# Kernel tuning notes

Hardware: AMD Instinct MI355X
Metric: run time of the kernel (lower is better)

The kernel has to match this reference:

```python
import jax, jax.numpy as jnp
import numpy as np

NUM_HEADS = 32
NUM_KV_HEADS = 8
NUM_GROUPS = NUM_HEADS // NUM_KV_HEADS  # 4
HEAD_DIM = 64
HIDDEN = 2048
ROPE_THETA = 10000.0


def rotate_half(x):
    half = x.shape[-1] // 2
    x1, x2 = x[..., :half], x[..., half:]
    return jnp.concatenate([-x2, x1], axis=-1)


def rope_cos_sin(seq_len, dtype):
    inv_freq = 1.0 / (ROPE_THETA ** (jnp.arange(0, HEAD_DIM, 2, dtype=jnp.float32) / HEAD_DIM))
    pos = jnp.arange(seq_len, dtype=jnp.float32)
    freqs = jnp.outer(pos, inv_freq)          # [S, HEAD_DIM/2]
    emb = jnp.concatenate([freqs, freqs], axis=-1)  # [S, HEAD_DIM]
    return jnp.cos(emb).astype(dtype), jnp.sin(emb).astype(dtype)


def setup_inputs() -> dict:
    key = jax.random.key(0)
    k0, k1, k2, k3, k4 = jax.random.split(key, 5)
    B, S = 2, 2048
    scale = 0.02
    return {
        "hidden_states": jax.random.normal(k0, (B, S, HIDDEN), dtype=jnp.float32),
        "Wq": jax.random.normal(k1, (NUM_HEADS * HEAD_DIM, HIDDEN), dtype=jnp.float32) * scale,
        "Wk": jax.random.normal(k2, (NUM_KV_HEADS * HEAD_DIM, HIDDEN), dtype=jnp.float32) * scale,
        "Wv": jax.random.normal(k3, (NUM_KV_HEADS * HEAD_DIM, HIDDEN), dtype=jnp.float32) * scale,
        "Wo": jax.random.normal(k4, (HIDDEN, NUM_HEADS * HEAD_DIM), dtype=jnp.float32) * scale,
    }


def reference(hidden_states, Wq, Wk, Wv, Wo):
    B, S, _ = hidden_states.shape
    # projections (nn.Linear: x @ W.T)
    q = (hidden_states @ Wq.T).reshape(B, S, NUM_HEADS, HEAD_DIM).transpose(0, 2, 1, 3)
    k = (hidden_states @ Wk.T).reshape(B, S, NUM_KV_HEADS, HEAD_DIM).transpose(0, 2, 1, 3)
    v = (hidden_states @ Wv.T).reshape(B, S, NUM_KV_HEADS, HEAD_DIM).transpose(0, 2, 1, 3)

    cos, sin = rope_cos_sin(S, q.dtype)  # [S, HEAD_DIM]
    cos = cos[None, None]                # [1,1,S,HEAD_DIM]
    sin = sin[None, None]
    q = q * cos + rotate_half(q) * sin
    k = k * cos + rotate_half(k) * sin

    # GQA: repeat kv heads to match query heads (repeat_interleave on head dim)
    k = jnp.repeat(k, NUM_GROUPS, axis=1)  # [B, NUM_HEADS, S, HEAD_DIM]
    v = jnp.repeat(v, NUM_GROUPS, axis=1)

    scale = 1.0 / jnp.sqrt(jnp.asarray(HEAD_DIM, dtype=q.dtype))
    scores = jnp.einsum('bhqd,bhkd->bhqk', q, k) * scale  # [B,H,S,S]
    causal = jnp.tril(jnp.ones((S, S), dtype=bool))
    scores = jnp.where(causal[None, None], scores, jnp.asarray(-jnp.inf, dtype=scores.dtype))
    attn = jax.nn.softmax(scores, axis=-1)
    out = jnp.einsum('bhqk,bhkd->bhqd', attn, v)           # [B,H,S,D]
    out = out.transpose(0, 2, 1, 3).reshape(B, S, NUM_HEADS * HEAD_DIM)
    return out @ Wo.T
```

## Files before the change

### kernel.cpp

```cpp
#include <hip/hip_runtime.h>

#define S_LEN 2048
#define BATCH 2
#define NH 32
#define NKV 8
#define HD 64
#define HID 2048
#define NTOK (BATCH * S_LEN)
#define NQKV 3072
#define SC_Q 0.18033688011112042f

typedef __attribute__((ext_vector_type(8))) __bf16 bf16x8;
typedef __attribute__((ext_vector_type(4))) float f32x4;

__device__ inline ushort f2b(float f) {
    union { float f; unsigned u; } x{f};
    unsigned r = (x.u + 0x7fff + ((x.u >> 16) & 1)) >> 16;
    return (ushort)r;
}
__device__ inline float b2f(ushort u) {
    union { unsigned u; float f; } x{(unsigned)u << 16};
    return x.f;
}
__device__ inline float ex2(float x) { return __builtin_amdgcn_exp2f(x); }

__global__ __launch_bounds__(256) void cvt_all(const float* __restrict__ hidden,
                                               const float* __restrict__ Wq,
                                               const float* __restrict__ Wk,
                                               const float* __restrict__ Wv,
                                               const float* __restrict__ Wo,
                                               ushort* __restrict__ hb,
                                               ushort* __restrict__ wqkv,
                                               ushort* __restrict__ wo) {
    int bid = blockIdx.x;
    const float* src;
    ushort* dst;
    int off;
    if (bid < 8192)        { src = hidden; dst = hb;                              off = bid; }
    else if (bid < 12288)  { src = Wq;     dst = wqkv;                            off = bid - 8192; }
    else if (bid < 13312)  { src = Wk;     dst = wqkv + (size_t)2048 * 2048;      off = bid - 12288; }
    else if (bid < 14336)  { src = Wv;     dst = wqkv + (size_t)2560 * 2048;      off = bid - 13312; }
    else                   { src = Wo;     dst = wo;                              off = bid - 14336; }
    size_t i = (size_t)off * 256 + threadIdx.x;
    float4 v = reinterpret_cast<const float4*>(src)[i];
    ushort4 o;
    o.x = f2b(v.x); o.y = f2b(v.y); o.z = f2b(v.z); o.w = f2b(v.w);
    reinterpret_cast<ushort4*>(dst)[i] = o;
}

__device__ inline void gl_lds16(const void* g, void* l) {
    __builtin_amdgcn_global_load_lds((const __attribute__((address_space(1))) void*)g,
                                     (__attribute__((address_space(3))) void*)l, 16, 0, 0);
}

template<int CF, int WF32, int ROUTE>
__global__ __launch_bounds__(512, 2) void gemm8p(const ushort* __restrict__ A,
                                                 const ushort* __restrict__ B,
                                                 void* __restrict__ C,
                                                 ushort* __restrict__ Kd,
                                                 ushort* __restrict__ Vd,
                                                 int M, int N, int K) {
    constexpr int BN = CF * 64;
    constexpr int ABYTES = 256 * 64 * 2;
    constexpr int BBYTES = BN * 64 * 2;
    __shared__ __align__(16) char lds[2][ABYTES + BBYTES];
    const int tid = threadIdx.x, lane = tid & 63, w = tid >> 6;
    const int wm = w >> 2, wn = w & 3, l15 = lane & 15, lg = lane >> 4;

    const int nbx = gridDim.x;
    int lid = blockIdx.y * nbx + blockIdx.x;
    const int cpx = (nbx * gridDim.y) >> 3;
    int swzb = (lid & 7) * cpx + (lid >> 3);
    const int m0 = (swzb / nbx) * 256, n0 = (swzb % nbx) * BN;

    const int srow = tid >> 3;
    const int scol = ((tid & 7) ^ (srow & 7)) * 8;
    const ushort* Ag = A + (size_t)(m0 + srow) * K + scol;
    const ushort* Bg = B + (size_t)(n0 + srow) * K + scol;

    auto stage = [&](int buf, int k0) {
        char* base = &lds[buf][0];
#pragma unroll
        for (int j = 0; j < 4; j++)
            gl_lds16(Ag + (size_t)(j * 64) * K + k0, base + (j * 64 + w * 8) * 128);
#pragma unroll
        for (int j = 0; j < CF; j++)
            gl_lds16(Bg + (size_t)(j * 64) * K + k0, base + ABYTES + (j * 64 + w * 8) * 128);
    };

    f32x4 acc[8][CF] = {};

    stage(0, 0);
    asm volatile("s_waitcnt vmcnt(0)" ::: "memory");
    __builtin_amdgcn_s_barrier();
    __builtin_amdgcn_sched_barrier(0);

    const int NT = K >> 6;
    const int sw = (l15 & 7) * 16;
    const int po0 = (lg * 16) ^ sw, po1 = (64 + lg * 16) ^ sw;

    for (int t = 0; t < NT; ++t) {
        const char* pa = &lds[t & 1][0] + (wm * 128 + l15) * 128;
        const char* pb = &lds[t & 1][ABYTES] + (wn * CF * 16 + l15) * 128;

        bf16x8 bf_[2][CF];
        bf16x8 a0[2][2];
#pragma unroll
        for (int j = 0; j < CF; j++) {
            bf_[0][j] = *(const bf16x8*)(pb + j * 2048 + po0);
            bf_[1][j] = *(const bf16x8*)(pb + j * 2048 + po1);
        }
#pragma unroll
        for (int i = 0; i < 2; i++) {
            a0[0][i] = *(const bf16x8*)(pa + i * 2048 + po0);
            a0[1][i] = *(const bf16x8*)(pa + i * 2048 + po1);
        }
        if (t + 1 < NT) stage((t + 1) & 1, (t + 1) << 6);
        __builtin_amdgcn_sched_barrier(0);
        __builtin_amdgcn_s_barrier();
        __builtin_amdgcn_sched_barrier(0);
        __builtin_amdgcn_s_setprio(1);
#pragma unroll
        for (int ks = 0; ks < 2; ks++)
#pragma unroll
            for (int i = 0; i < 2; i++)
#pragma unroll
                for (int j = 0; j < CF; j++)
                    acc[i][j] = __builtin_amdgcn_mfma_f32_16x16x32_bf16(a0[ks][i], bf_[ks][j], acc[i][j], 0, 0, 0);
        __builtin_amdgcn_s_setprio(0);

#pragma unroll
        for (int p = 1; p < 4; p++) {
            bf16x8 ap[2][2];
#pragma unroll
            for (int i = 0; i < 2; i++) {
                ap[0][i] = *(const bf16x8*)(pa + (p * 2 + i) * 2048 + po0);
                ap[1][i] = *(const bf16x8*)(pa + (p * 2 + i) * 2048 + po1);
            }
            __builtin_amdgcn_sched_barrier(0);
            __builtin_amdgcn_s_barrier();
            __builtin_amdgcn_sched_barrier(0);
            __builtin_amdgcn_s_setprio(1);
#pragma unroll
            for (int ks = 0; ks < 2; ks++)
#pragma unroll
                for (int i = 0; i < 2; i++)
#pragma unroll
                    for (int j = 0; j < CF; j++)
                        acc[p * 2 + i][j] = __builtin_amdgcn_mfma_f32_16x16x32_bf16(ap[ks][i], bf_[ks][j], acc[p * 2 + i][j], 0, 0, 0);
            __builtin_amdgcn_s_setprio(0);
        }

        asm volatile("s_waitcnt vmcnt(0)" ::: "memory");
        __builtin_amdgcn_s_barrier();
        __builtin_amdgcn_sched_barrier(0);
    }

    const int mr = m0 + wm * 128 + lg * 4;

    if (ROUTE) {
#pragma unroll
        for (int j = 0; j < CF; j++) {
            int cb = n0 + wn * CF * 16 + j * 16;
            ushort* dst;
            int dstride, colb;
            if (cb < 2048)      { dst = (ushort*)C; dstride = 2048; colb = cb + l15; }
            else if (cb < 2560) { dst = Kd;         dstride = 512;  colb = cb - 2048 + l15; }
            else                { dst = Vd;         dstride = 512;  colb = cb - 2560 + l15; }
#pragma unroll
            for (int i = 0; i < 8; i++)
#pragma unroll
                for (int r = 0; r < 4; r++)
                    dst[(size_t)(mr + i * 16 + r) * dstride + colb] = f2b(acc[i][j][r]);
        }
    } else {
#pragma unroll
        for (int i = 0; i < 8; i++)
#pragma unroll
            for (int j = 0; j < CF; j++)
#pragma unroll
                for (int r = 0; r < 4; r++) {
                    size_t row = mr + i * 16 + r, col = n0 + wn * CF * 16 + j * 16 + l15;
                    if (WF32) ((float*)C)[row * N + col] = acc[i][j][r];
                    else      ((ushort*)C)[row * N + col] = f2b(acc[i][j][r]);
                }
    }
}

__global__ __launch_bounds__(256) void rope_k(ushort* __restrict__ Qb, ushort* __restrict__ Kb) {
    int idx = blockIdx.x * 256 + threadIdx.x;
    int t = idx / 160, rem = idx - t * 160;
    int hh = rem >> 2, q8 = rem & 3;
    float pos = (float)(t & (S_LEN - 1));
    ushort* base = (hh < 32) ? Qb + (size_t)t * 2048 + hh * 64 + q8 * 8
                             : Kb + (size_t)t * 512 + (hh - 32) * 64 + q8 * 8;
    float sc = (hh < 32) ? SC_Q : 1.0f;
    ushort4 v0 = *(ushort4*)base, v1 = *(ushort4*)(base + 4);
    ushort4 u0 = *(ushort4*)(base + 32), u1 = *(ushort4*)(base + 36);
    ushort lo[8] = {v0.x, v0.y, v0.z, v0.w, v1.x, v1.y, v1.z, v1.w};
    ushort hi[8] = {u0.x, u0.y, u0.z, u0.w, u1.x, u1.y, u1.z, u1.w};
#pragma unroll
    for (int e = 0; e < 8; e++) {
        float f = ex2(-(float)(q8 * 8 + e) * 0.4152410118609203f);
        float sv, cv;
        __sincosf(pos * f, &sv, &cv);
        float x1 = b2f(lo[e]), x2 = b2f(hi[e]);
        lo[e] = f2b((x1 * cv - x2 * sv) * sc);
        hi[e] = f2b((x2 * cv + x1 * sv) * sc);
    }
    *(ushort4*)base        = make_ushort4(lo[0], lo[1], lo[2], lo[3]);
    *(ushort4*)(base + 4)  = make_ushort4(lo[4], lo[5], lo[6], lo[7]);
    *(ushort4*)(base + 32) = make_ushort4(hi[0], hi[1], hi[2], hi[3]);
    *(ushort4*)(base + 36) = make_ushort4(hi[4], hi[5], hi[6], hi[7]);
}

__global__ __launch_bounds__(256) void transpose_v(const ushort* __restrict__ V,
                                                   ushort* __restrict__ Vt) {
    __shared__ ushort tile[32][33];
    int bz = blockIdx.z, b = bz >> 3, kvh = bz & 7;
    int s0 = blockIdx.x * 32, d0 = blockIdx.y * 32;
    int tx = threadIdx.x & 31, ty = threadIdx.x >> 5;
#pragma unroll
    for (int i = 0; i < 4; i++)
        tile[ty + i * 8][tx] = V[(size_t)(b * S_LEN + s0 + ty + i * 8) * 512 + kvh * 64 + d0 + tx];
    __syncthreads();
#pragma unroll
    for (int i = 0; i < 4; i++)
        Vt[((size_t)((b * 8 + kvh) * 64 + d0 + ty + i * 8)) * S_LEN + s0 + tx] = tile[tx][ty + i * 8];
}

__global__ __launch_bounds__(256) void attn_k(const ushort* __restrict__ Q,
                                              const ushort* __restrict__ Kc,
                                              const ushort* __restrict__ Vt,
                                              ushort* __restrict__ O) {
    __shared__ __align__(16) ushort K_lds[3][4096];
    __shared__ __align__(16) ushort V_lds[3][4096];
    const int lane = threadIdx.x & 63, w = threadIdx.x >> 6;
    const int l15 = lane & 15, lg = lane >> 4;

    int lid = blockIdx.y * 8 + blockIdx.x;
    int swz = (lid & 7) * 64 + (lid >> 3);
    const int ps = swz & 7;
    const int bh = swz >> 3;
    const int b = bh >> 5, h = bh & 31, kvh = h >> 2;

    const ushort* kSrc[2];
    const ushort* vSrc[2];
    int dstU[2];
#pragma unroll
    for (int j = 0; j < 2; j++) {
        int u = w * 2 + j;
        int row = u * 8 + (lane >> 3);
        int po = (lane & 7) * 16;
        int fr = ((row & 3) | (((row >> 3) & 1) << 2)) << 4;
        int dus = (po ^ fr) >> 1;
        kSrc[j] = Kc + (size_t)(b * S_LEN + row) * 512 + kvh * 64 + dus;
        vSrc[j] = Vt + ((size_t)((b * 8 + kvh) * 64 + row)) * S_LEN + dus;
        dstU[j] = u * 512;
    }

    int fr_k = ((l15 & 3) | (((l15 >> 2) & 1) << 2)) << 4;
    int kbase = 1024 * (l15 >> 2) + 128 * (l15 & 3) + ((lg * 16) ^ (fr_k & 48));
    int k6 = (fr_k >> 6) & 1;
    int kb0 = kbase + 64 * k6, kb1 = kbase + 64 * (1 - k6);
    int fr_v = ((l15 & 3) | (((l15 >> 3) & 1) << 2)) << 4;
    int vbase = 128 * l15 + ((lg * 16) ^ (fr_v & 48));
    int v6 = (fr_v >> 6) & 1;
    int vb0 = vbase + 64 * v6, vb1 = vbase + 64 * (1 - v6);

    bf16x8 onesf;
#pragma unroll
    for (int i = 0; i < 8; i++) onesf[i] = (__bf16)1.0f;

    for (int half = 0; half < 2; ++half) {
        const int pp = half ? (15 - ps) : ps;
        const int q0A = pp * 128 + w * 16, q0B = q0A + 64;
        const int qrowA = q0A + l15, qrowB = q0B + l15;
        const int ktA = 2 * pp, ktB = 2 * pp + 1;

        const ushort* qpA = Q + (size_t)(b * S_LEN + qrowA) * HID + h * 64 + lg * 8;
        const ushort* qpB = Q + (size_t)(b * S_LEN + qrowB) * HID + h * 64 + lg * 8;
        bf16x8 qfA0 = *(const bf16x8*)qpA, qfA1 = *(const bf16x8*)(qpA + 32);
        bf16x8 qfB0 = *(const bf16x8*)qpB, qfB1 = *(const bf16x8*)(qpB + 32);
        asm volatile("s_waitcnt vmcnt(0)" ::: "memory");

        f32x4 aoA[4] = {}, aoB[4] = {};
        f32x4 lsumA = {}, lsumB = {};

        int i0 = 0, i1 = 1, i2 = 2;
#pragma unroll
        for (int j = 0; j < 2; j++) {
            gl_lds16(kSrc[j], &K_lds[0][dstU[j]]);
            gl_lds16(vSrc[j], &V_lds[0][dstU[j]]);
        }
#pragma unroll
        for (int j = 0; j < 2; j++) {
            gl_lds16(kSrc[j] + (size_t)64 * 512, &K_lds[1][dstU[j]]);
            gl_lds16(vSrc[j] + 64, &V_lds[1][dstU[j]]);
        }

        for (int kt = 0; kt <= ktB; ++kt) {
            const int kn = kt << 6;
            if (kt < ktB) asm volatile("s_waitcnt vmcnt(4)" ::: "memory");
            else          asm volatile("s_waitcnt vmcnt(0)" ::: "memory");
            __builtin_amdgcn_s_barrier();

            if (kt + 2 <= ktB) {
                const int kn2 = kn + 128;
#pragma unroll
                for (int j = 0; j < 2; j++) {
                    gl_lds16(kSrc[j] + (size_t)kn2 * 512, &K_lds[i2][dstU[j]]);
                    gl_lds16(vSrc[j] + kn2, &V_lds[i2][dstU[j]]);
                }
            }

            const char* Kt = (const char*)&K_lds[i0][0];
            const char* Vl = (const char*)&V_lds[i0][0];
            const bool aAct = (kt <= ktA);

            bf16x8 kf0[4], kf1[4];
#pragma unroll
            for (int kc = 0; kc < 4; kc++) {
                const int kcst = 4096 * (kc >> 1) + 512 * (kc & 1);
                kf0[kc] = *(const bf16x8*)(Kt + kb0 + kcst);
                kf1[kc] = *(const bf16x8*)(Kt + kb1 + kcst);
            }

            f32x4 sB[4], sA[4];
#pragma unroll
            for (int kc = 0; kc < 4; kc++) {
                f32x4 z = {};
                z = __builtin_amdgcn_mfma_f32_16x16x32_bf16(kf0[kc], qfB0, z, 0, 0, 0);
                z = __builtin_amdgcn_mfma_f32_16x16x32_bf16(kf1[kc], qfB1, z, 0, 0, 0);
                sB[kc] = z;
            }
            if (aAct) {
#pragma unroll
                for (int kc = 0; kc < 4; kc++) {
                    f32x4 z = {};
                    z = __builtin_amdgcn_mfma_f32_16x16x32_bf16(kf0[kc], qfA0, z, 0, 0, 0);
                    z = __builtin_amdgcn_mfma_f32_16x16x32_bf16(kf1[kc], qfA1, z, 0, 0, 0);
                    sA[kc] = z;
                }
            }

            if (kt == ktB) {
#pragma unroll
                for (int kc = 0; kc < 4; kc++)
#pragma unroll
                    for (int r = 0; r < 4; r++) {
                        int kv = kn + ((kc >> 1) << 5) + (lg << 3) + ((kc & 1) << 2) + r;
                        sB[kc][r] = (kv <= qrowB) ? sB[kc][r] : -INFINITY;
                    }
            }
            if (kt == ktA) {
#pragma unroll
                for (int kc = 0; kc < 4; kc++)
#pragma unroll
                    for (int r = 0; r < 4; r++) {
                        int kv = kn + ((kc >> 1) << 5) + (lg << 3) + ((kc & 1) << 2) + r;
                        sA[kc][r] = (kv <= qrowA) ? sA[kc][r] : -INFINITY;
                    }
            }

            bf16x8 pB0, pB1, pA0, pA1;
#pragma unroll
            for (int r = 0; r < 4; r++) {
                pB0[r]     = (__bf16)ex2(sB[0][r]);
                pB0[4 + r] = (__bf16)ex2(sB[1][r]);
                pB1[r]     = (__bf16)ex2(sB[2][r]);
                pB1[4 + r] = (__bf16)ex2(sB[3][r]);
            }
            if (aAct) {
#pragma unroll
                for (int r = 0; r < 4; r++) {
                    pA0[r]     = (__bf16)ex2(sA[0][r]);
                    pA0[4 + r] = (__bf16)ex2(sA[1][r]);
                    pA1[r]     = (__bf16)ex2(sA[2][r]);
                    pA1[4 + r] = (__bf16)ex2(sA[3][r]);
                }
            }

            lsumB = __builtin_amdgcn_mfma_f32_16x16x32_bf16(pB0, onesf, lsumB, 0, 0, 0);
            lsumB = __builtin_amdgcn_mfma_f32_16x16x32_bf16(pB1, onesf, lsumB, 0, 0, 0);
            if (aAct) {
                lsumA = __builtin_amdgcn_mfma_f32_16x16x32_bf16(pA0, onesf, lsumA, 0, 0, 0);
                lsumA = __builtin_amdgcn_mfma_f32_16x16x32_bf16(pA1, onesf, lsumA, 0, 0, 0);
            }

#pragma unroll
            for (int dt = 0; dt < 4; dt++) {
                bf16x8 vf0 = *(const bf16x8*)(Vl + vb0 + dt * 2048);
                bf16x8 vf1 = *(const bf16x8*)(Vl + vb1 + dt * 2048);
                aoB[dt] = __builtin_amdgcn_mfma_f32_16x16x32_bf16(pB0, vf0, aoB[dt], 0, 0, 0);
                aoB[dt] = __builtin_amdgcn_mfma_f32_16x16x32_bf16(pB1, vf1, aoB[dt], 0, 0, 0);
                if (aAct) {
                    aoA[dt] = __builtin_amdgcn_mfma_f32_16x16x32_bf16(pA0, vf0, aoA[dt], 0, 0, 0);
                    aoA[dt] = __builtin_amdgcn_mfma_f32_16x16x32_bf16(pA1, vf1, aoA[dt], 0, 0, 0);
                }
            }

            int t = i0; i0 = i1; i1 = i2; i2 = t;
        }

        float invA[4], invB[4];
#pragma unroll
        for (int r = 0; r < 4; r++) { invA[r] = 1.0f / lsumA[r]; invB[r] = 1.0f / lsumB[r]; }
        ushort* obA = O + (size_t)(b * S_LEN + q0A + lg * 4) * HID + h * 64 + l15;
        ushort* obB = O + (size_t)(b * S_LEN + q0B + lg * 4) * HID + h * 64 + l15;
#pragma unroll
        for (int dt = 0; dt < 4; dt++)
#pragma unroll
            for (int r = 0; r < 4; r++) {
                union { __bf16 h; ushort u; } cA{(__bf16)(aoA[dt][r] * invA[r])};
                union { __bf16 h; ushort u; } cB{(__bf16)(aoB[dt][r] * invB[r])};
                obA[(size_t)r * HID + dt * 16] = cA.u;
                obB[(size_t)r * HID + dt * 16] = cB.u;
            }

        __builtin_amdgcn_s_barrier();
    }
}

extern "C" void kernel_launch(void* const* d_in, const int* in_sizes, int n_in,
                              void* d_out, int out_size, void* d_ws, size_t ws_size,
                              hipStream_t stream) {
    const float* hidden = (const float*)d_in[0];
    const float* Wq = (const float*)d_in[1];
    const float* Wk = (const float*)d_in[2];
    const float* Wv = (const float*)d_in[3];
    const float* Wo = (const float*)d_in[4];

    char* ws = (char*)d_ws;
    size_t off = 0;
    auto alloc = [&](size_t bytes) -> void* {
        void* p = ws + off;
        off += (bytes + 255) & ~(size_t)255;
        return p;
    };
    ushort* hb   = (ushort*)alloc((size_t)NTOK * HID * 2);
    ushort* wqkv = (ushort*)alloc((size_t)NQKV * 2048 * 2);
    ushort* wo   = (ushort*)alloc((size_t)2048 * 2048 * 2);
    ushort* Qb   = (ushort*)alloc((size_t)NTOK * 2048 * 2);
    ushort* Kb   = (ushort*)alloc((size_t)NTOK * 512 * 2);
    ushort* Vb   = (ushort*)alloc((size_t)NTOK * 512 * 2);
    ushort* Vtb  = (ushort*)alloc((size_t)NTOK * 512 * 2);
    ushort* AO   = (ushort*)alloc((size_t)NTOK * 2048 * 2);

    cvt_all<<<18432, 256, 0, stream>>>(hidden, Wq, Wk, Wv, Wo, hb, wqkv, wo);

    gemm8p<3, 0, 1><<<dim3(16, 16), 512, 0, stream>>>(hb, wqkv, Qb, Kb, Vb, NTOK, NQKV, 2048);

    rope_k<<<(NTOK * 40 * 4) / 256, 256, 0, stream>>>(Qb, Kb);

    transpose_v<<<dim3(S_LEN / 32, 2, BATCH * NKV), 256, 0, stream>>>(Vb, Vtb);

    attn_k<<<dim3(8, BATCH * NH), 256, 0, stream>>>(Qb, Kb, Vtb, AO);

    gemm8p<2, 1, 0><<<dim3(16, 16), 512, 0, stream>>>(AO, wo, d_out, nullptr, nullptr, NTOK, 2048, 2048);
}
```

Before: 164.5 us.

## Restructure GEMM pipeline, fuse Q RoPE into attention, grid-stride conversion kernel

The GEMM main loop now issues the next tile's loads at the start of each iteration and uses partial vmcnt waits, replacing four barrier-separated MFMA phases with two. A-row loads are reordered to match. Q RoPE and scaling move from the standalone rope kernel into the attention kernel's Q load, so the rope kernel only rewrites K and Q makes one less round trip through memory. The fp32-to-bf16 conversion kernel becomes a grid-stride loop with nontemporal loads over fewer blocks. The risks are fragile vmcnt counts tied to the load order and extra sincos work repeated per attention block.

Result: no change. 164.3 us (-0.1%).

```diff
diff --git a/kernel.cpp b/kernel.cpp
--- a/kernel.cpp
+++ b/kernel.cpp
@@ -12,6 +12,8 @@
 
 typedef __attribute__((ext_vector_type(8))) __bf16 bf16x8;
 typedef __attribute__((ext_vector_type(4))) float f32x4;
+typedef __attribute__((ext_vector_type(4))) float f32x4v;
+typedef __attribute__((ext_vector_type(4))) ushort u16x4;
 
 __device__ inline ushort f2b(float f) {
     union { float f; unsigned u; } x{f};
@@ -32,20 +34,20 @@
                                                ushort* __restrict__ hb,
                                                ushort* __restrict__ wqkv,
                                                ushort* __restrict__ wo) {
-    int bid = blockIdx.x;
-    const float* src;
-    ushort* dst;
-    int off;
-    if (bid < 8192)        { src = hidden; dst = hb;                              off = bid; }
-    else if (bid < 12288)  { src = Wq;     dst = wqkv;                            off = bid - 8192; }
-    else if (bid < 13312)  { src = Wk;     dst = wqkv + (size_t)2048 * 2048;      off = bid - 12288; }
-    else if (bid < 14336)  { src = Wv;     dst = wqkv + (size_t)2560 * 2048;      off = bid - 13312; }
-    else                   { src = Wo;     dst = wo;                              off = bid - 14336; }
-    size_t i = (size_t)off * 256 + threadIdx.x;
-    float4 v = reinterpret_cast<const float4*>(src)[i];
-    ushort4 o;
-    o.x = f2b(v.x); o.y = f2b(v.y); o.z = f2b(v.z); o.w = f2b(v.w);
-    reinterpret_cast<ushort4*>(dst)[i] = o;
+    for (int bid = blockIdx.x; bid < 18432; bid += gridDim.x) {
+        const float* src;
+        ushort* dst;
+        int off;
+        if (bid < 8192)        { src = hidden; dst = hb;                              off = bid; }
+        else if (bid < 12288)  { src = Wq;     dst = wqkv;                            off = bid - 8192; }
+        else if (bid < 13312)  { src = Wk;     dst = wqkv + (size_t)2048 * 2048;      off = bid - 12288; }
+        else if (bid < 14336)  { src = Wv;     dst = wqkv + (size_t)2560 * 2048;      off = bid - 13312; }
+        else                   { src = Wo;     dst = wo;                              off = bid - 14336; }
+        size_t i = (size_t)off * 256 + threadIdx.x;
+        f32x4v v = __builtin_nontemporal_load((const f32x4v*)src + i);
+        u16x4 o = {f2b(v[0]), f2b(v[1]), f2b(v[2]), f2b(v[3])};
+        *((u16x4*)dst + i) = o;
+    }
 }
 
 __device__ inline void gl_lds16(const void* g, void* l) {
@@ -81,19 +83,17 @@
     auto stage = [&](int buf, int k0) {
         char* base = &lds[buf][0];
 #pragma unroll
-        for (int j = 0; j < 4; j++)
-            gl_lds16(Ag + (size_t)(j * 64) * K + k0, base + (j * 64 + w * 8) * 128);
-#pragma unroll
         for (int j = 0; j < CF; j++)
             gl_lds16(Bg + (size_t)(j * 64) * K + k0, base + ABYTES + (j * 64 + w * 8) * 128);
+        gl_lds16(Ag + k0,                      base + (0 * 64 + w * 8) * 128);
+        gl_lds16(Ag + (size_t)(2 * 64) * K + k0, base + (2 * 64 + w * 8) * 128);
+        gl_lds16(Ag + (size_t)(1 * 64) * K + k0, base + (1 * 64 + w * 8) * 128);
+        gl_lds16(Ag + (size_t)(3 * 64) * K + k0, base + (3 * 64 + w * 8) * 128);
     };
 
     f32x4 acc[8][CF] = {};
 
     stage(0, 0);
-    asm volatile("s_waitcnt vmcnt(0)" ::: "memory");
-    __builtin_amdgcn_s_barrier();
-    __builtin_amdgcn_sched_barrier(0);
 
     const int NT = K >> 6;
     const int sw = (l15 & 7) * 16;
@@ -103,57 +103,58 @@
         const char* pa = &lds[t & 1][0] + (wm * 128 + l15) * 128;
         const char* pb = &lds[t & 1][ABYTES] + (wn * CF * 16 + l15) * 128;
 
+        asm volatile("s_waitcnt vmcnt(2)" ::: "memory");
+        __builtin_amdgcn_s_barrier();
+        __builtin_amdgcn_sched_barrier(0);
+        if (t + 1 < NT) stage((t + 1) & 1, (t + 1) << 6);
+        __builtin_amdgcn_sched_barrier(0);
+
         bf16x8 bf_[2][CF];
-        bf16x8 a0[2][2];
 #pragma unroll
         for (int j = 0; j < CF; j++) {
             bf_[0][j] = *(const bf16x8*)(pb + j * 2048 + po0);
             bf_[1][j] = *(const bf16x8*)(pb + j * 2048 + po1);
         }
-#pragma unroll
-        for (int i = 0; i < 2; i++) {
-            a0[0][i] = *(const bf16x8*)(pa + i * 2048 + po0);
-            a0[1][i] = *(const bf16x8*)(pa + i * 2048 + po1);
-        }
-        if (t + 1 < NT) stage((t + 1) & 1, (t + 1) << 6);
-        __builtin_amdgcn_sched_barrier(0);
+        bf16x8 a_[2][4];
+#pragma unroll
+        for (int i = 0; i < 4; i++) {
+            a_[0][i] = *(const bf16x8*)(pa + i * 2048 + po0);
+            a_[1][i] = *(const bf16x8*)(pa + i * 2048 + po1);
+        }
+        __builtin_amdgcn_s_setprio(1);
+#pragma unroll
+        for (int ks = 0; ks < 2; ks++)
+#pragma unroll
+            for (int i = 0; i < 4; i++)
+#pragma unroll
+                for (int j = 0; j < CF; j++)
+                    acc[i][j] = __builtin_amdgcn_mfma_f32_16x16x32_bf16(a_[ks][i], bf_[ks][j], acc[i][j], 0, 0, 0);
+        __builtin_amdgcn_s_setprio(0);
+
+        if (t < NT - 1) {
+            if constexpr (CF == 3) asm volatile("s_waitcnt vmcnt(7)" ::: "memory");
+            else                   asm volatile("s_waitcnt vmcnt(6)" ::: "memory");
+        } else {
+            asm volatile("s_waitcnt vmcnt(0)" ::: "memory");
+        }
         __builtin_amdgcn_s_barrier();
         __builtin_amdgcn_sched_barrier(0);
+
+        bf16x8 c_[2][4];
+#pragma unroll
+        for (int i = 0; i < 4; i++) {
+            c_[0][i] = *(const bf16x8*)(pa + (4 + i) * 2048 + po0);
+            c_[1][i] = *(const bf16x8*)(pa + (4 + i) * 2048 + po1);
+        }
         __builtin_amdgcn_s_setprio(1);
 #pragma unroll
         for (int ks = 0; ks < 2; ks++)
 #pragma unroll
-            for (int i = 0; i < 2; i++)
+            for (int i = 0; i < 4; i++)
 #pragma unroll
                 for (int j = 0; j < CF; j++)
-                    acc[i][j] = __builtin_amdgcn_mfma_f32_16x16x32_bf16(a0[ks][i], bf_[ks][j], acc[i][j], 0, 0, 0);
+                    acc[4 + i][j] = __builtin_amdgcn_mfma_f32_16x16x32_bf16(c_[ks][i], bf_[ks][j], acc[4 + i][j], 0, 0, 0);
         __builtin_amdgcn_s_setprio(0);
-
-#pragma unroll
-        for (int p = 1; p < 4; p++) {
-            bf16x8 ap[2][2];
-#pragma unroll
-            for (int i = 0; i < 2; i++) {
-                ap[0][i] = *(const bf16x8*)(pa + (p * 2 + i) * 2048 + po0);
-                ap[1][i] = *(const bf16x8*)(pa + (p * 2 + i) * 2048 + po1);
-            }
-            __builtin_amdgcn_sched_barrier(0);
-            __builtin_amdgcn_s_barrier();
-            __builtin_amdgcn_sched_barrier(0);
-            __builtin_amdgcn_s_setprio(1);
-#pragma unroll
-            for (int ks = 0; ks < 2; ks++)
-#pragma unroll
-                for (int i = 0; i < 2; i++)
-#pragma unroll
-                    for (int j = 0; j < CF; j++)
-                        acc[p * 2 + i][j] = __builtin_amdgcn_mfma_f32_16x16x32_bf16(ap[ks][i], bf_[ks][j], acc[p * 2 + i][j], 0, 0, 0);
-            __builtin_amdgcn_s_setprio(0);
-        }
-
-        asm volatile("s_waitcnt vmcnt(0)" ::: "memory");
-        __builtin_amdgcn_s_barrier();
-        __builtin_amdgcn_sched_barrier(0);
     }
 
     const int mr = m0 + wm * 128 + lg * 4;
@@ -187,14 +188,12 @@
     }
 }
 
-__global__ __launch_bounds__(256) void rope_k(ushort* __restrict__ Qb, ushort* __restrict__ Kb) {
+__global__ __launch_bounds__(256) void rope_k(ushort* __restrict__ Kb) {
     int idx = blockIdx.x * 256 + threadIdx.x;
-    int t = idx / 160, rem = idx - t * 160;
+    int t = idx >> 5, rem = idx & 31;
     int hh = rem >> 2, q8 = rem & 3;
     float pos = (float)(t & (S_LEN - 1));
-    ushort* base = (hh < 32) ? Qb + (size_t)t * 2048 + hh * 64 + q8 * 8
-                             : Kb + (size_t)t * 512 + (hh - 32) * 64 + q8 * 8;
-    float sc = (hh < 32) ? SC_Q : 1.0f;
+    ushort* base = Kb + (size_t)t * 512 + hh * 64 + q8 * 8;
     ushort4 v0 = *(ushort4*)base, v1 = *(ushort4*)(base + 4);
     ushort4 u0 = *(ushort4*)(base + 32), u1 = *(ushort4*)(base + 36);
     ushort lo[8] = {v0.x, v0.y, v0.z, v0.w, v1.x, v1.y, v1.z, v1.w};
@@ -205,8 +204,8 @@
         float sv, cv;
         __sincosf(pos * f, &sv, &cv);
         float x1 = b2f(lo[e]), x2 = b2f(hi[e]);
-        lo[e] = f2b((x1 * cv - x2 * sv) * sc);
-        hi[e] = f2b((x2 * cv + x1 * sv) * sc);
+        lo[e] = f2b(x1 * cv - x2 * sv);
+        hi[e] = f2b(x2 * cv + x1 * sv);
     }
     *(ushort4*)base        = make_ushort4(lo[0], lo[1], lo[2], lo[3]);
     *(ushort4*)(base + 4)  = make_ushort4(lo[4], lo[5], lo[6], lo[7]);
@@ -272,6 +271,19 @@
 #pragma unroll
     for (int i = 0; i < 8; i++) onesf[i] = (__bf16)1.0f;
 
+    auto ropeq = [&](bf16x8& q0, bf16x8& q1, int qrow) {
+        float pos = (float)qrow;
+#pragma unroll
+        for (int e = 0; e < 8; e++) {
+            float f = ex2(-(float)(lg * 8 + e) * 0.4152410118609203f);
+            float sv, cv;
+            __sincosf(pos * f, &sv, &cv);
+            float x1 = (float)q0[e], x2 = (float)q1[e];
+            q0[e] = (__bf16)((x1 * cv - x2 * sv) * SC_Q);
+            q1[e] = (__bf16)((x2 * cv + x1 * sv) * SC_Q);
+        }
+    };
+
     for (int half = 0; half < 2; ++half) {
         const int pp = half ? (15 - ps) : ps;
         const int q0A = pp * 128 + w * 16, q0B = q0A + 64;
@@ -282,6 +294,8 @@
         const ushort* qpB = Q + (size_t)(b * S_LEN + qrowB) * HID + h * 64 + lg * 8;
         bf16x8 qfA0 = *(const bf16x8*)qpA, qfA1 = *(const bf16x8*)(qpA + 32);
         bf16x8 qfB0 = *(const bf16x8*)qpB, qfB1 = *(const bf16x8*)(qpB + 32);
+        ropeq(qfA0, qfA1, qrowA);
+        ropeq(qfB0, qfB1, qrowB);
         asm volatile("s_waitcnt vmcnt(0)" ::: "memory");
 
         f32x4 aoA[4] = {}, aoB[4] = {};
@@ -447,11 +461,11 @@
     ushort* Vtb  = (ushort*)alloc((size_t)NTOK * 512 * 2);
     ushort* AO   = (ushort*)alloc((size_t)NTOK * 2048 * 2);
 
-    cvt_all<<<18432, 256, 0, stream>>>(hidden, Wq, Wk, Wv, Wo, hb, wqkv, wo);
+    cvt_all<<<2304, 256, 0, stream>>>(hidden, Wq, Wk, Wv, Wo, hb, wqkv, wo);
 
     gemm8p<3, 0, 1><<<dim3(16, 16), 512, 0, stream>>>(hb, wqkv, Qb, Kb, Vb, NTOK, NQKV, 2048);
 
-    rope_k<<<(NTOK * 40 * 4) / 256, 256, 0, stream>>>(Qb, Kb);
+    rope_k<<<(NTOK * 32) / 256, 256, 0, stream>>>(Kb);
 
     transpose_v<<<dim3(S_LEN / 32, 2, BATCH * NKV), 256, 0, stream>>>(Vb, Vtb);
 
```
